# Kernel tuning notes

Hardware: AMD Instinct MI355X
Metric: run time of the kernel (lower is better)

Reference implementation:

```python
import jax, jax.numpy as jnp
from jax import lax
import numpy as np

B, C, L = 8, 64, 32768
K = 4
DEPTH = 8


def _causal_depthwise_conv(x, weight, dilation):
    # x: [B, C, L], weight: [C, 1, K] depthwise (groups=C). stride=1 so the
    # torch pad formula reduces to left-pad dilation*(K-1), output length L.
    pad = dilation * (K - 1)
    return lax.conv_general_dilated(
        x, weight,
        window_strides=(1,),
        padding=[(pad, 0)],
        rhs_dilation=(dilation,),
        dimension_numbers=("NCH", "OIH", "NCH"),
        feature_group_count=C,
    )


def setup_inputs() -> dict:
    key = jax.random.key(0)
    k1, k2, k3, k4 = jax.random.split(key, 4)
    scalar = np.sqrt(2.0 / (K * 2)).astype(np.float32)
    w_scale = np.sqrt(2.0 / (2 * DEPTH + 4)).astype(np.float32)
    return {
        "x": jax.random.normal(k1, (B, C, L), dtype=jnp.float32),
        "h0": jax.random.uniform(k2, (C, 1, K), minval=-1.0, maxval=1.0, dtype=jnp.float32) * scalar,
        "h1": jax.random.uniform(k3, (C, 1, K), minval=-1.0, maxval=1.0, dtype=jnp.float32) * scalar,
        "w": jax.random.uniform(k4, (C, DEPTH + 2), minval=-1.0, maxval=1.0, dtype=jnp.float32) * w_scale,
    }


def reference(x, h0, h1, w):
    residual_low = x
    y = jnp.zeros_like(x)
    dilation = 1
    for i in range(DEPTH, 0, -1):
        residual_high = _causal_depthwise_conv(residual_low, h1, dilation)
        residual_low = _causal_depthwise_conv(residual_low, h0, dilation)
        y = y + w[:, i][None, :, None] * residual_high
        dilation *= 2
    y = y + w[:, 0][None, :, None] * residual_low
    y = y + x * w[:, -1][None, :, None]
    # dropout p=0 is identity; torch GELU default is exact (erf)
    return jax.nn.gelu(y, approximate=False)
```

## Files before the change

kernel.cpp:

```cpp
#include <hip/hip_runtime.h>
#include <cmath>

namespace {

typedef _Float16 h8 __attribute__((ext_vector_type(8)));
typedef _Float16 h2 __attribute__((ext_vector_type(2)));
typedef __fp16   fp2 __attribute__((ext_vector_type(2)));

constexpr int C_     = 64;
constexpr int L_     = 32768;
constexpr int TILE   = 2048;
constexpr int HALO   = 776;
constexpr int NB     = TILE + HALO;
constexpr int NU     = NB / 8;
constexpr int HALO_U = HALO / 8;
constexpr int NT     = L_ / TILE;
constexpr int BLK    = 128;
constexpr int UMAX   = (NU + BLK - 1) / BLK;

__device__ __forceinline__ h8 ld8(const _Float16* p) { return *reinterpret_cast<const h8*>(p); }
__device__ __forceinline__ void st8(_Float16* p, h8 v) { *reinterpret_cast<h8*>(p) = v; }
__device__ __forceinline__ float4 ld4f(const float* p) { return *reinterpret_cast<const float4*>(p); }
__device__ __forceinline__ void st4f(float* p, float4 v) { *reinterpret_cast<float4*>(p) = v; }
__device__ __forceinline__ h8 sp8(_Float16 v) { return (h8){v,v,v,v,v,v,v,v}; }

__device__ __forceinline__ h8 fma8(h8 a, h8 b, h8 c) {
    return __builtin_elementwise_fma(a, b, c);
}

template<int K>
__device__ __forceinline__ h8 shconc(h8 A, h8 B) {
    return __builtin_shufflevector(A, B, K, K+1, K+2, K+3, K+4, K+5, K+6, K+7);
}

__device__ __forceinline__ h2 pkrtz(float lo, float hi) {
    const fp2 r = __builtin_amdgcn_cvt_pkrtz(lo, hi);
    return __builtin_bit_cast(h2, r);
}
__device__ __forceinline__ h8 pack8(float4 a, float4 b) {
    const h2 p0 = pkrtz(a.x, a.y);
    const h2 p1 = pkrtz(a.z, a.w);
    const h2 p2 = pkrtz(b.x, b.y);
    const h2 p3 = pkrtz(b.z, b.w);
    return (h8){p0[0], p0[1], p1[0], p1[1], p2[0], p2[1], p3[0], p3[1]};
}

__device__ __forceinline__ float gelu_f(float v) {
    const float z = v * (1.5957691216057308f + 0.0713548162726f * v * v);
    const float e = __expf(-z);
    return v * __builtin_amdgcn_rcpf(1.0f + e);
}

template<int D, int STARTU, bool LAST>
__device__ __forceinline__ void level_pass(const _Float16* __restrict__ src,
                                           _Float16* __restrict__ dst,
                                           const float* h0f, const float* h1f,
                                           float wi, float w0,
                                           h8* lw, h8* yacc, int tid)
{
    _Float16 c1[4], c0[4];
#pragma unroll
    for (int t = 0; t < 4; ++t) {
        c1[t] = (_Float16)(wi * h1f[t]);
        c0[t] = (_Float16)(LAST ? w0 * h0f[t] : h0f[t]);
    }

#pragma unroll
    for (int u = 0; u < UMAX; ++u) {
        const int un = tid + u * BLK;
        if (un >= STARTU && un < NU) {
            const int p = 8 * un;
            const h8 T3 = lw[u];
            h8 T0, T1, T2;
            if constexpr (D == 1) {
                h8 Lv = ld8(&src[p - 8]);
                T0 = shconc<5>(Lv, T3);
                T1 = shconc<6>(Lv, T3);
                T2 = shconc<7>(Lv, T3);
            } else if constexpr (D == 2) {
                h8 Lv = ld8(&src[p - 8]);
                T0 = shconc<2>(Lv, T3);
                T1 = shconc<4>(Lv, T3);
                T2 = shconc<6>(Lv, T3);
            } else if constexpr (D == 4) {
                h8 Lv  = ld8(&src[p - 8]);
                h8 LL  = ld8(&src[p - 16]);
                T0 = shconc<4>(LL, Lv);
                T1 = Lv;
                T2 = shconc<4>(Lv, T3);
            } else {
                T0 = ld8(&src[p - 3 * D]);
                T1 = ld8(&src[p - 2 * D]);
                T2 = ld8(&src[p - D]);
            }
            if (un >= HALO_U) {
                h8 yv = yacc[u];
                yv = fma8(sp8(c1[0]), T0, yv);
                yv = fma8(sp8(c1[1]), T1, yv);
                yv = fma8(sp8(c1[2]), T2, yv);
                yv = fma8(sp8(c1[3]), T3, yv);
                yacc[u] = yv;
            }
            h8 nl = sp8(c0[0]) * T0;
            nl = fma8(sp8(c0[1]), T1, nl);
            nl = fma8(sp8(c0[2]), T2, nl);
            nl = fma8(sp8(c0[3]), T3, nl);
            if constexpr (LAST) {
                yacc[u] += nl;
            } else {
                lw[u] = nl;
                st8(&dst[p], nl);
            }
        }
    }
}

__global__ __launch_bounds__(BLK, 8)
void cmrc_kernel(const float* __restrict__ x,
                 const float* __restrict__ h0,
                 const float* __restrict__ h1,
                 const float* __restrict__ w,
                 float* __restrict__ out)
{
    __shared__ alignas(16) _Float16 buf[2][NB];

    const int tid  = threadIdx.x;
    const int blk  = blockIdx.x;
    const int tile = blk % NT;
    const int bc   = blk / NT;
    const int c    = bc % C_;
    const long row = (long)bc * L_;
    const int  t0  = tile * TILE - HALO;

    float h0v[4], h1v[4];
#pragma unroll
    for (int k = 0; k < 4; ++k) { h0v[k] = h0[c*4+k]; h1v[k] = h1[c*4+k]; }
    float wv[10];
#pragma unroll
    for (int i = 0; i < 10; ++i) wv[i] = w[c*10+i];

    h8 lw[UMAX];
    h8 yacc[UMAX];

    const _Float16 w9h = (_Float16)wv[9];

#pragma unroll
    for (int u = 0; u < UMAX; ++u) {
        yacc[u] = sp8((_Float16)0.f);
        const int un = tid + u * BLK;
        if (un < NU) {
            const int p = 8 * un;
            const int t = t0 + p;
            float4 xa = make_float4(0.f, 0.f, 0.f, 0.f);
            float4 xb = make_float4(0.f, 0.f, 0.f, 0.f);
            if (t >= 0) { xa = ld4f(&x[row + t]); xb = ld4f(&x[row + t + 4]); }
            const h8 hv = pack8(xa, xb);
            st8(&buf[0][p], hv);
            lw[u] = hv;
            if (un >= HALO_U) yacc[u] = sp8(w9h) * hv;
        }
    }
    __syncthreads();

    level_pass<1,   1,  false>(buf[0], buf[1], h0v, h1v, wv[8], 0.f, lw, yacc, tid); __syncthreads();
    level_pass<2,   2,  false>(buf[1], buf[0], h0v, h1v, wv[7], 0.f, lw, yacc, tid); __syncthreads();
    level_pass<4,   4,  false>(buf[0], buf[1], h0v, h1v, wv[6], 0.f, lw, yacc, tid); __syncthreads();
    level_pass<8,   7,  false>(buf[1], buf[0], h0v, h1v, wv[5], 0.f, lw, yacc, tid); __syncthreads();
    level_pass<16,  13, false>(buf[0], buf[1], h0v, h1v, wv[4], 0.f, lw, yacc, tid); __syncthreads();
    level_pass<32,  25, false>(buf[1], buf[0], h0v, h1v, wv[3], 0.f, lw, yacc, tid); __syncthreads();
    level_pass<64,  49, false>(buf[0], buf[1], h0v, h1v, wv[2], 0.f, lw, yacc, tid); __syncthreads();
    level_pass<128, 97, true >(buf[1], buf[0], h0v, h1v, wv[1], wv[0], lw, yacc, tid);

#pragma unroll
    for (int u = 0; u < UMAX; ++u) {
        const int un = tid + u * BLK;
        if (un >= HALO_U && un < NU) {
            const int p = 8 * un;
            const h8 v = yacc[u];
            float4 oa, ob;
            oa.x = gelu_f((float)v[0]); oa.y = gelu_f((float)v[1]);
            oa.z = gelu_f((float)v[2]); oa.w = gelu_f((float)v[3]);
            ob.x = gelu_f((float)v[4]); ob.y = gelu_f((float)v[5]);
            ob.z = gelu_f((float)v[6]); ob.w = gelu_f((float)v[7]);
            st4f(&out[row + t0 + p], oa);
            st4f(&out[row + t0 + p + 4], ob);
        }
    }
}

}

extern "C" void kernel_launch(void* const* d_in, const int* in_sizes, int n_in,
                              void* d_out, int out_size, void* d_ws, size_t ws_size,
                              hipStream_t stream)
{
    const float* x  = (const float*)d_in[0];
    const float* h0 = (const float*)d_in[1];
    const float* h1 = (const float*)d_in[2];
    const float* w  = (const float*)d_in[3];
    float* out = (float*)d_out;

    const int nblocks = (out_size / L_) * NT;
    cmrc_kernel<<<nblocks, BLK, 0, stream>>>(x, h0, h1, w, out);
}
```

Baseline: 46.91 us.

## Double tile length and block size, specialize per-thread unit schedule

Doubles the sequence tile to 4096 with 256 threads per block, so the fixed 776-element causal halo is recomputed over a larger useful region and there are fewer blocks. The generic unrolled loop is replaced by three explicit unit steps per thread, running the always-full middle unit first and guarding only the partial and halo units. Filter weights are converted to half precision once up front rather than multiplying in float each level. Risks include lower occupancy from doubled shared memory per block (about 9.7KB), fewer blocks to fill the GPU, and slightly different rounding from forming the coefficient products in half precision.

```diff
diff --git a/kernel.cpp b/kernel.cpp
--- a/kernel.cpp
+++ b/kernel.cpp
@@ -9,14 +9,14 @@
 
 constexpr int C_     = 64;
 constexpr int L_     = 32768;
-constexpr int TILE   = 2048;
+constexpr int TILE   = 4096;
 constexpr int HALO   = 776;
 constexpr int NB     = TILE + HALO;
 constexpr int NU     = NB / 8;
 constexpr int HALO_U = HALO / 8;
 constexpr int NT     = L_ / TILE;
-constexpr int BLK    = 128;
-constexpr int UMAX   = (NU + BLK - 1) / BLK;
+constexpr int BLK    = 256;
+constexpr int S2N    = NU - 2 * BLK;
 
 __device__ __forceinline__ h8 ld8(const _Float16* p) { return *reinterpret_cast<const h8*>(p); }
 __device__ __forceinline__ void st8(_Float16* p, h8 v) { *reinterpret_cast<h8*>(p) = v; }
@@ -51,68 +51,68 @@
     return v * __builtin_amdgcn_rcpf(1.0f + e);
 }
 
+template<int D, bool LAST>
+__device__ __forceinline__ void unit_step(const _Float16* __restrict__ src,
+                                          _Float16* __restrict__ dst, int un,
+                                          h8& lwv, h8& yv, bool doY,
+                                          const _Float16* c1, const _Float16* c0)
+{
+    const int p = 8 * un;
+    const h8 T3 = lwv;
+    h8 T0, T1, T2;
+    if constexpr (D == 1) {
+        const h8 Lv = ld8(&src[p - 8]);
+        T0 = shconc<5>(Lv, T3); T1 = shconc<6>(Lv, T3); T2 = shconc<7>(Lv, T3);
+    } else if constexpr (D == 2) {
+        const h8 Lv = ld8(&src[p - 8]);
+        T0 = shconc<2>(Lv, T3); T1 = shconc<4>(Lv, T3); T2 = shconc<6>(Lv, T3);
+    } else if constexpr (D == 4) {
+        const h8 Lv = ld8(&src[p - 8]);
+        const h8 LL = ld8(&src[p - 16]);
+        T0 = shconc<4>(LL, Lv); T1 = Lv; T2 = shconc<4>(Lv, T3);
+    } else {
+        T0 = ld8(&src[p - 3 * D]);
+        T1 = ld8(&src[p - 2 * D]);
+        T2 = ld8(&src[p - D]);
+    }
+    if (doY) {
+        h8 yt = yv;
+        yt = fma8(sp8(c1[0]), T0, yt);
+        yt = fma8(sp8(c1[1]), T1, yt);
+        yt = fma8(sp8(c1[2]), T2, yt);
+        yt = fma8(sp8(c1[3]), T3, yt);
+        yv = yt;
+    }
+    h8 nl = sp8(c0[0]) * T0;
+    nl = fma8(sp8(c0[1]), T1, nl);
+    nl = fma8(sp8(c0[2]), T2, nl);
+    nl = fma8(sp8(c0[3]), T3, nl);
+    if constexpr (LAST) {
+        yv += nl;
+    } else {
+        lwv = nl;
+        st8(&dst[p], nl);
+    }
+}
+
 template<int D, int STARTU, bool LAST>
 __device__ __forceinline__ void level_pass(const _Float16* __restrict__ src,
                                            _Float16* __restrict__ dst,
-                                           const float* h0f, const float* h1f,
-                                           float wi, float w0,
+                                           const _Float16* h0h, const _Float16* h1h,
+                                           _Float16 wih, _Float16 w0h,
                                            h8* lw, h8* yacc, int tid)
 {
     _Float16 c1[4], c0[4];
 #pragma unroll
     for (int t = 0; t < 4; ++t) {
-        c1[t] = (_Float16)(wi * h1f[t]);
-        c0[t] = (_Float16)(LAST ? w0 * h0f[t] : h0f[t]);
-    }
-
-#pragma unroll
-    for (int u = 0; u < UMAX; ++u) {
-        const int un = tid + u * BLK;
-        if (un >= STARTU && un < NU) {
-            const int p = 8 * un;
-            const h8 T3 = lw[u];
-            h8 T0, T1, T2;
-            if constexpr (D == 1) {
-                h8 Lv = ld8(&src[p - 8]);
-                T0 = shconc<5>(Lv, T3);
-                T1 = shconc<6>(Lv, T3);
-                T2 = shconc<7>(Lv, T3);
-            } else if constexpr (D == 2) {
-                h8 Lv = ld8(&src[p - 8]);
-                T0 = shconc<2>(Lv, T3);
-                T1 = shconc<4>(Lv, T3);
-                T2 = shconc<6>(Lv, T3);
-            } else if constexpr (D == 4) {
-                h8 Lv  = ld8(&src[p - 8]);
-                h8 LL  = ld8(&src[p - 16]);
-                T0 = shconc<4>(LL, Lv);
-                T1 = Lv;
-                T2 = shconc<4>(Lv, T3);
-            } else {
-                T0 = ld8(&src[p - 3 * D]);
-                T1 = ld8(&src[p - 2 * D]);
-                T2 = ld8(&src[p - D]);
-            }
-            if (un >= HALO_U) {
-                h8 yv = yacc[u];
-                yv = fma8(sp8(c1[0]), T0, yv);
-                yv = fma8(sp8(c1[1]), T1, yv);
-                yv = fma8(sp8(c1[2]), T2, yv);
-                yv = fma8(sp8(c1[3]), T3, yv);
-                yacc[u] = yv;
-            }
-            h8 nl = sp8(c0[0]) * T0;
-            nl = fma8(sp8(c0[1]), T1, nl);
-            nl = fma8(sp8(c0[2]), T2, nl);
-            nl = fma8(sp8(c0[3]), T3, nl);
-            if constexpr (LAST) {
-                yacc[u] += nl;
-            } else {
-                lw[u] = nl;
-                st8(&dst[p], nl);
-            }
-        }
-    }
+        c1[t] = wih * h1h[t];
+        c0[t] = LAST ? (_Float16)(w0h * h0h[t]) : h0h[t];
+    }
+    unit_step<D, LAST>(src, dst, tid + BLK, lw[1], yacc[1], true, c1, c0);
+    if (tid < S2N)
+        unit_step<D, LAST>(src, dst, tid + 2 * BLK, lw[2], yacc[2], true, c1, c0);
+    if (tid >= STARTU)
+        unit_step<D, LAST>(src, dst, tid, lw[0], yacc[0], tid >= HALO_U, c1, c0);
 }
 
 __global__ __launch_bounds__(BLK, 8)
@@ -132,20 +132,21 @@
     const long row = (long)bc * L_;
     const int  t0  = tile * TILE - HALO;
 
-    float h0v[4], h1v[4];
-#pragma unroll
-    for (int k = 0; k < 4; ++k) { h0v[k] = h0[c*4+k]; h1v[k] = h1[c*4+k]; }
-    float wv[10];
-#pragma unroll
-    for (int i = 0; i < 10; ++i) wv[i] = w[c*10+i];
-
-    h8 lw[UMAX];
-    h8 yacc[UMAX];
-
-    const _Float16 w9h = (_Float16)wv[9];
-
-#pragma unroll
-    for (int u = 0; u < UMAX; ++u) {
+    _Float16 h0h[4], h1h[4];
+#pragma unroll
+    for (int k = 0; k < 4; ++k) {
+        h0h[k] = (_Float16)h0[c * 4 + k];
+        h1h[k] = (_Float16)h1[c * 4 + k];
+    }
+    _Float16 wh[10];
+#pragma unroll
+    for (int i = 0; i < 10; ++i) wh[i] = (_Float16)w[c * 10 + i];
+
+    h8 lw[3];
+    h8 yacc[3];
+
+#pragma unroll
+    for (int u = 0; u < 3; ++u) {
         yacc[u] = sp8((_Float16)0.f);
         const int un = tid + u * BLK;
         if (un < NU) {
@@ -157,22 +158,22 @@
             const h8 hv = pack8(xa, xb);
             st8(&buf[0][p], hv);
             lw[u] = hv;
-            if (un >= HALO_U) yacc[u] = sp8(w9h) * hv;
+            if (un >= HALO_U) yacc[u] = sp8(wh[9]) * hv;
         }
     }
     __syncthreads();
 
-    level_pass<1,   1,  false>(buf[0], buf[1], h0v, h1v, wv[8], 0.f, lw, yacc, tid); __syncthreads();
-    level_pass<2,   2,  false>(buf[1], buf[0], h0v, h1v, wv[7], 0.f, lw, yacc, tid); __syncthreads();
-    level_pass<4,   4,  false>(buf[0], buf[1], h0v, h1v, wv[6], 0.f, lw, yacc, tid); __syncthreads();
-    level_pass<8,   7,  false>(buf[1], buf[0], h0v, h1v, wv[5], 0.f, lw, yacc, tid); __syncthreads();
-    level_pass<16,  13, false>(buf[0], buf[1], h0v, h1v, wv[4], 0.f, lw, yacc, tid); __syncthreads();
-    level_pass<32,  25, false>(buf[1], buf[0], h0v, h1v, wv[3], 0.f, lw, yacc, tid); __syncthreads();
-    level_pass<64,  49, false>(buf[0], buf[1], h0v, h1v, wv[2], 0.f, lw, yacc, tid); __syncthreads();
-    level_pass<128, 97, true >(buf[1], buf[0], h0v, h1v, wv[1], wv[0], lw, yacc, tid);
-
-#pragma unroll
-    for (int u = 0; u < UMAX; ++u) {
+    level_pass<1,   1,  false>(buf[0], buf[1], h0h, h1h, wh[8], (_Float16)0.f, lw, yacc, tid); __syncthreads();
+    level_pass<2,   2,  false>(buf[1], buf[0], h0h, h1h, wh[7], (_Float16)0.f, lw, yacc, tid); __syncthreads();
+    level_pass<4,   4,  false>(buf[0], buf[1], h0h, h1h, wh[6], (_Float16)0.f, lw, yacc, tid); __syncthreads();
+    level_pass<8,   7,  false>(buf[1], buf[0], h0h, h1h, wh[5], (_Float16)0.f, lw, yacc, tid); __syncthreads();
+    level_pass<16,  13, false>(buf[0], buf[1], h0h, h1h, wh[4], (_Float16)0.f, lw, yacc, tid); __syncthreads();
+    level_pass<32,  25, false>(buf[1], buf[0], h0h, h1h, wh[3], (_Float16)0.f, lw, yacc, tid); __syncthreads();
+    level_pass<64,  49, false>(buf[0], buf[1], h0h, h1h, wh[2], (_Float16)0.f, lw, yacc, tid); __syncthreads();
+    level_pass<128, 97, true >(buf[1], buf[0], h0h, h1h, wh[1], wh[0],         lw, yacc, tid);
+
+#pragma unroll
+    for (int u = 0; u < 3; ++u) {
         const int un = tid + u * BLK;
         if (un >= HALO_U && un < NU) {
             const int p = 8 * un;
```

After: 42.23 us. 1.11x faster.
